# Kernel optimization log

Hardware: AMD Instinct MI355X
Metric: run time of the kernel (lower is better)

## Reference

```python
import jax, jax.numpy as jnp
import numpy as np

B, S, T, DIN, H, DOUT = 64, 256, 256, 128, 1024, 128
TEACHER_FORCING_RATIO = 0.0  # deterministic reference: always feed back own prediction


def setup_inputs() -> dict:
    key = jax.random.key(0)
    ks = jax.random.split(key, 12)
    bound = 1.0 / np.sqrt(H)
    u = lambda k, sh: jax.random.uniform(k, sh, jnp.float32, -bound, bound)
    return {
        "src": jax.random.normal(ks[0], (B, S, DIN), jnp.float32),
        "trg": jax.random.normal(ks[1], (B, T, DOUT), jnp.float32),
        "enc_Wih": u(ks[2], (4 * H, DIN)),
        "enc_Whh": u(ks[3], (4 * H, H)),
        "enc_bih": u(ks[4], (4 * H,)),
        "enc_bhh": u(ks[5], (4 * H,)),
        "dec_Wih": u(ks[6], (4 * H, DOUT)),
        "dec_Whh": u(ks[7], (4 * H, H)),
        "dec_bih": u(ks[8], (4 * H,)),
        "dec_bhh": u(ks[9], (4 * H,)),
        "fc_W": u(ks[10], (DOUT, H)),
        "fc_b": u(ks[11], (DOUT,)),
    }


def _lstm_cell(x_t, h, c, Wih, Whh, b):
    # PyTorch gate order: i, f, g, o
    gates = x_t @ Wih.T + h @ Whh.T + b  # [B, 4H]
    i, f, g, o = jnp.split(gates, 4, axis=-1)
    c = jax.nn.sigmoid(f) * c + jax.nn.sigmoid(i) * jnp.tanh(g)
    h = jax.nn.sigmoid(o) * jnp.tanh(c)
    return h, c


def _encode(src, Wih, Whh, b):
    Bn = src.shape[0]
    Hn = Whh.shape[1]
    h0 = jnp.zeros((Bn, Hn), src.dtype)
    c0 = jnp.zeros((Bn, Hn), src.dtype)

    def step(carry, xt):
        h, c = carry
        h, c = _lstm_cell(xt, h, c, Wih, Whh, b)
        return (h, c), None

    (h, c), _ = jax.lax.scan(step, (h0, c0), jnp.swapaxes(src, 0, 1))
    return h, c


def reference(src, trg, enc_Wih, enc_Whh, enc_bih, enc_bhh,
              dec_Wih, dec_Whh, dec_bih, dec_bhh, fc_W, fc_b):
    Bn, Tn, Dn = trg.shape
    h, c = _encode(src, enc_Wih, enc_Whh, enc_bih + enc_bhh)
    db = dec_bih + dec_bhh

    def step(carry, _):
        h, c, inp = carry
        h, c = _lstm_cell(inp, h, c, dec_Wih, dec_Whh, db)
        pred = h @ fc_W.T + fc_b  # [B, DOUT]
        # teacher_forcing_ratio = 0.0 -> next input is own prediction
        return (h, c, pred), pred

    _, preds = jax.lax.scan(step, (h, c, trg[:, 0, :]), None, length=Tn - 1)
    preds = jnp.swapaxes(preds, 0, 1)  # [B, T-1, DOUT]
    # outputs[:, 0, :] stays zero, as in the original
    return jnp.concatenate([jnp.zeros((Bn, 1, Dn), trg.dtype), preds], axis=1)
```

## Files before the change

### kernel.cpp

```cpp
#include <hip/hip_runtime.h>


#define BB   64
#define HH   1024
#define G4   4096
#define DXX  128
#define KC   128
#define SEQN 256
#define TN   256
#define OUT_BSTRIDE (TN * DXX)

#define HROW 2048
#define SLOT (64 * HROW)

typedef __attribute__((ext_vector_type(8))) short short8;
typedef __attribute__((ext_vector_type(4))) float f32x4;

__device__ __forceinline__ float sigm(float x)  { return 1.f / (1.f + __expf(-x)); }
__device__ __forceinline__ float tanh_f(float x){ return 1.f - 2.f / (1.f + __expf(2.f * x)); }

__device__ __forceinline__ unsigned short bf16_rn(float x) {
    union { float f; unsigned u; } v; v.f = x;
    unsigned r = v.u + 0x7fffu + ((v.u >> 16) & 1u);
    return (unsigned short)(r >> 16);
}
__device__ __forceinline__ float bf16f(unsigned short h) {
    union { unsigned u; float f; } v; v.u = ((unsigned)h) << 16; return v.f;
}

template<int KT, bool XPART>
__device__ __forceinline__ void do_step(
    const short8 (&w)[9][2],
    const unsigned short* __restrict__ A,
    unsigned short* __restrict__ An,
    float* red, int mrow, int kl, int kw, int rbase,
    int t, int b, int nl, int nh, const float (&bb)[4], float& creg,
    const unsigned short* __restrict__ xs,
    unsigned* __restrict__ bar, unsigned step)
{
    f32x4 acc = {0.f, 0.f, 0.f, 0.f};
    const unsigned short* Ar = A + mrow * HROW;
    #pragma unroll
    for (int kt = 0; kt < KT; ++kt) {
        const int kg = kw * (KT * 32) + kt * 32 + kl;
        short8 ah, al;
        if (XPART && kw == 3 && kt >= 5) {
            const int xo = mrow * 256 + (kg - 1024);
            ah = *(const short8*)(xs + xo);
            al = *(const short8*)(xs + xo + 128);
        } else {
            ah = *(const short8*)(Ar + kg);
            al = *(const short8*)(Ar + 1024 + kg);
        }
        acc = __builtin_amdgcn_mfma_f32_16x16x32_bf16(ah, w[kt][0], acc, 0, 0, 0);
        acc = __builtin_amdgcn_mfma_f32_16x16x32_bf16(ah, w[kt][1], acc, 0, 0, 0);
        acc = __builtin_amdgcn_mfma_f32_16x16x32_bf16(al, w[kt][0], acc, 0, 0, 0);
    }
    #pragma unroll
    for (int r = 0; r < 4; ++r) red[rbase + r * 17] = acc[r];
    __syncthreads();

    if (t < 256) {
        float g4[4];
        #pragma unroll
        for (int gt = 0; gt < 4; ++gt) {
            const int cc = nl * 4 + gt;
            g4[gt] = red[b * 17 + cc] + red[(64 + b) * 17 + cc]
                   + red[(128 + b) * 17 + cc] + red[(192 + b) * 17 + cc] + bb[gt];
        }
        const float cv = sigm(g4[1]) * creg + sigm(g4[0]) * tanh_f(g4[2]);
        creg = cv;
        const float hv = sigm(g4[3]) * tanh_f(cv);
        const unsigned short hh = bf16_rn(hv);
        const unsigned short hl = bf16_rn(hv - bf16f(hh));
        const unsigned phh = (unsigned)__shfl_xor((int)(unsigned)hh, 1);
        const unsigned phl = (unsigned)__shfl_xor((int)(unsigned)hl, 1);
        if ((nl & 1) == 0) {
            const unsigned wh = (unsigned)hh | (phh << 16);
            const unsigned wl = (unsigned)hl | (phl << 16);
            __hip_atomic_store((unsigned*)(An + b * HROW + nh), wh,
                               __ATOMIC_RELAXED, __HIP_MEMORY_SCOPE_AGENT);
            __hip_atomic_store((unsigned*)(An + b * HROW + 1024 + nh), wl,
                               __ATOMIC_RELAXED, __HIP_MEMORY_SCOPE_AGENT);
        }
    }
    __syncthreads();
    if (t == 0)
        __hip_atomic_store(bar + blockIdx.x, step,
                           __ATOMIC_RELAXED, __HIP_MEMORY_SCOPE_AGENT);
    if (blockIdx.x == 0) {
        if (t < 64) {
            const unsigned* sp = bar + t * 4;
            for (;;) {
                const unsigned m0 = __hip_atomic_load(sp + 0, __ATOMIC_RELAXED, __HIP_MEMORY_SCOPE_AGENT);
                const unsigned m1 = __hip_atomic_load(sp + 1, __ATOMIC_RELAXED, __HIP_MEMORY_SCOPE_AGENT);
                const unsigned m2 = __hip_atomic_load(sp + 2, __ATOMIC_RELAXED, __HIP_MEMORY_SCOPE_AGENT);
                const unsigned m3 = __hip_atomic_load(sp + 3, __ATOMIC_RELAXED, __HIP_MEMORY_SCOPE_AGENT);
                const bool ok = (m0 >= step) & (m1 >= step) & (m2 >= step) & (m3 >= step);
                if (__all((int)ok)) break;
                __builtin_amdgcn_s_sleep(1);
            }
            if (t < 16)
                __hip_atomic_store(bar + 256 + t * 32, step,
                                   __ATOMIC_RELAXED, __HIP_MEMORY_SCOPE_AGENT);
        }
    } else if (t == 0) {
        const unsigned* ep = bar + 256 + (blockIdx.x & 15) * 32;
        while (__hip_atomic_load(ep, __ATOMIC_RELAXED,
                                 __HIP_MEMORY_SCOPE_AGENT) < step)
            __builtin_amdgcn_s_sleep(1);
    }
    __syncthreads();
}

__global__ __launch_bounds__(1024, 1)
void persist(const unsigned short* __restrict__ Wencf,
             const unsigned short* __restrict__ Wdec0f,
             const unsigned short* __restrict__ Wcombf,
             const unsigned short* __restrict__ srcp,
             const unsigned short* __restrict__ trgp,
             const float* __restrict__ benc,
             const float* __restrict__ bdec0,
             const float* __restrict__ bcomb,
             unsigned short* __restrict__ hseq,
             unsigned* __restrict__ bar)
{
    __shared__ float red[4 * 64 * 17];
    const int t  = threadIdx.x;
    const int bi = blockIdx.x;
    const int l  = t & 63;
    const int wv = t >> 6;
    const int mw = wv & 3;
    const int kw = wv >> 2;
    const int lm = l & 15;
    const int kl = (l >> 4) << 3;
    const int mrow = mw * 16 + lm;
    const int rbase = (kw * 64 + mw * 16 + (l >> 4) * 4) * 17 + lm;
    const int b  = t >> 2;
    const int nl = t & 3;
    const int nh = bi * 4 + nl;

    short8 w[9][2];
    float bb[4];
    float creg = 0.f;
    unsigned step = 0;

    {
        const unsigned short* wp = Wencf + ((size_t)(bi * 4 + kw) * 9) * 1024 + l * 8;
        #pragma unroll
        for (int kt = 0; kt < 9; ++kt) {
            w[kt][0] = *(const short8*)(wp + kt * 1024);
            w[kt][1] = *(const short8*)(wp + kt * 1024 + 512);
            asm volatile("" : "+v"(w[kt][0]), "+v"(w[kt][1]));
        }
    }
    if (t < 256) {
        #pragma unroll
        for (int g = 0; g < 4; ++g) bb[g] = benc[bi * 16 + nl * 4 + g];
    }
    for (int s = 0; s < 256; ++s) {
        ++step;
        do_step<9, true>(w, hseq + (size_t)s * SLOT, hseq + (size_t)(s + 1) * SLOT,
                         red, mrow, kl, kw, rbase, t, b, nl, nh, bb, creg,
                         srcp + (size_t)s * 16384, bar, step);
    }
    {
        const unsigned short* wp = Wdec0f + ((size_t)(bi * 4 + kw) * 9) * 1024 + l * 8;
        #pragma unroll
        for (int kt = 0; kt < 9; ++kt) {
            w[kt][0] = *(const short8*)(wp + kt * 1024);
            w[kt][1] = *(const short8*)(wp + kt * 1024 + 512);
            asm volatile("" : "+v"(w[kt][0]), "+v"(w[kt][1]));
        }
    }
    if (t < 256) {
        #pragma unroll
        for (int g = 0; g < 4; ++g) bb[g] = bdec0[bi * 16 + nl * 4 + g];
    }
    ++step;
    do_step<9, true>(w, hseq + (size_t)256 * SLOT, hseq + (size_t)257 * SLOT,
                     red, mrow, kl, kw, rbase, t, b, nl, nh, bb, creg,
                     trgp, bar, step);
    {
        const unsigned short* wp = Wcombf + ((size_t)(bi * 4 + kw) * 8) * 1024 + l * 8;
        #pragma unroll
        for (int kt = 0; kt < 8; ++kt) {
            w[kt][0] = *(const short8*)(wp + kt * 1024);
            w[kt][1] = *(const short8*)(wp + kt * 1024 + 512);
            asm volatile("" : "+v"(w[kt][0]), "+v"(w[kt][1]));
        }
    }
    if (t < 256) {
        #pragma unroll
        for (int g = 0; g < 4; ++g) bb[g] = bcomb[bi * 16 + nl * 4 + g];
    }
    for (int s = 257; s < 511; ++s) {
        ++step;
        do_step<8, false>(w, hseq + (size_t)s * SLOT, hseq + (size_t)(s + 1) * SLOT,
                          red, mrow, kl, kw, rbase, t, b, nl, nh, bb, creg,
                          nullptr, bar, step);
    }
}

__global__ __launch_bounds__(256)
void fc_batch(const unsigned short* __restrict__ fcf,
              const unsigned short* __restrict__ hseq,
              const float* __restrict__ fcb,
              float* __restrict__ out)
{
    const int t = threadIdx.x, bi = blockIdx.x;
    const int l = t & 63, wv = t >> 6;
    const int lm = l & 15, kl = (l >> 4) << 3;
    const int mrow = wv * 16 + lm;
    const unsigned short* Ar = hseq + (size_t)(257 + bi) * SLOT + mrow * HROW;

    f32x4 acc[8];
    #pragma unroll
    for (int nt = 0; nt < 8; ++nt) acc[nt] = f32x4{0.f, 0.f, 0.f, 0.f};

    for (int kt = 0; kt < 32; ++kt) {
        const short8 ah = *(const short8*)(Ar + kt * 32 + kl);
        const short8 al = *(const short8*)(Ar + 1024 + kt * 32 + kl);
        #pragma unroll
        for (int nt = 0; nt < 8; ++nt) {
            const unsigned short* bp = fcf + (size_t)(nt * 32 + kt) * 1024 + l * 8;
            const short8 bh = *(const short8*)bp;
            const short8 bl = *(const short8*)(bp + 512);
            acc[nt] = __builtin_amdgcn_mfma_f32_16x16x32_bf16(ah, bh, acc[nt], 0, 0, 0);
            acc[nt] = __builtin_amdgcn_mfma_f32_16x16x32_bf16(ah, bl, acc[nt], 0, 0, 0);
            acc[nt] = __builtin_amdgcn_mfma_f32_16x16x32_bf16(al, bh, acc[nt], 0, 0, 0);
        }
    }
    #pragma unroll
    for (int nt = 0; nt < 8; ++nt) {
        const float bv = fcb[nt * 16 + lm];
        #pragma unroll
        for (int r = 0; r < 4; ++r) {
            const int bq = wv * 16 + (l >> 4) * 4 + r;
            out[(size_t)bq * OUT_BSTRIDE + (size_t)(bi + 1) * DXX + nt * 16 + lm] = acc[nt][r] + bv;
        }
    }
}

__global__ __launch_bounds__(256)
void prep_frag_12(const float* __restrict__ Whh, const float* __restrict__ Wih,
                  unsigned short* __restrict__ dst)
{
    const int idx = blockIdx.x * 256 + threadIdx.x;
    const int l = idx & 63;
    const int fid = idx >> 6;
    const int kt = fid % 9;
    const int rem = fid / 9;
    const int kw = rem & 3;
    const int biq = rem >> 2;
    const int col = biq * 16 + (l & 15);
    const int hid = col >> 2, g = col & 3;
    const int k0 = kw * 288 + kt * 32 + ((l >> 4) << 3);
    short8 vh, vl;
    #pragma unroll
    for (int e = 0; e < 8; ++e) {
        const int k = k0 + e;
        const float wv = (k < 1024) ? Whh[(size_t)(g * 1024 + hid) * 1024 + k]
                                    : Wih[(size_t)(g * 1024 + hid) * 128 + (k - 1024)];
        const unsigned short hi = bf16_rn(wv);
        vh[e] = (short)hi;
        vl[e] = (short)bf16_rn(wv - bf16f(hi));
    }
    *(short8*)(dst + (size_t)fid * 1024 + l * 8) = vh;
    *(short8*)(dst + (size_t)fid * 1024 + 512 + l * 8) = vl;
}

__global__ __launch_bounds__(256)
void prep_frag_comb(const float* __restrict__ Wc, unsigned short* __restrict__ dst)
{
    const int idx = blockIdx.x * 256 + threadIdx.x;
    const int l = idx & 63;
    const int fid = idx >> 6;
    const int kt = fid & 7;
    const int rem = fid >> 3;
    const int kw = rem & 3;
    const int biq = rem >> 2;
    const int col = biq * 16 + (l & 15);
    const int hid = col >> 2, g = col & 3;
    const int k0 = kw * 256 + kt * 32 + ((l >> 4) << 3);
    short8 vh, vl;
    #pragma unroll
    for (int e = 0; e < 8; ++e) {
        const float wv = Wc[(size_t)(g * 1024 + hid) * 1024 + k0 + e];
        const unsigned short hi = bf16_rn(wv);
        vh[e] = (short)hi;
        vl[e] = (short)bf16_rn(wv - bf16f(hi));
    }
    *(short8*)(dst + (size_t)fid * 1024 + l * 8) = vh;
    *(short8*)(dst + (size_t)fid * 1024 + 512 + l * 8) = vl;
}

__global__ __launch_bounds__(256)
void prep_frag_fc(const float* __restrict__ fcW, unsigned short* __restrict__ dst)
{
    const int idx = blockIdx.x * 256 + threadIdx.x;
    const int l = idx & 63;
    const int fid = idx >> 6;
    const int nt = fid >> 5, kt = fid & 31;
    const int col = nt * 16 + (l & 15);
    const int k0 = kt * 32 + ((l >> 4) << 3);
    short8 vh, vl;
    #pragma unroll
    for (int e = 0; e < 8; ++e) {
        const float wv = fcW[(size_t)col * 1024 + k0 + e];
        const unsigned short hi = bf16_rn(wv);
        vh[e] = (short)hi;
        vl[e] = (short)bf16_rn(wv - bf16f(hi));
    }
    *(short8*)(dst + (size_t)fid * 1024 + l * 8) = vh;
    *(short8*)(dst + (size_t)fid * 1024 + 512 + l * 8) = vl;
}

__global__ __launch_bounds__(256)
void prep_bias_p(const float* __restrict__ ebi, const float* __restrict__ ebh,
                 const float* __restrict__ dbi, const float* __restrict__ dbh,
                 const float* __restrict__ dWih, const float* __restrict__ fcb,
                 float* __restrict__ benc, float* __restrict__ bdec0,
                 float* __restrict__ bcomb)
{
    const int idx = blockIdx.x * 256 + threadIdx.x;
    const int orig = ((idx & 3) << 10) | (idx >> 2);
    benc[idx] = ebi[orig] + ebh[orig];
    const float db = dbi[orig] + dbh[orig];
    bdec0[idx] = db;
    float a = db;
    const float* wr = dWih + (size_t)orig * DXX;
    for (int d = 0; d < DXX; ++d) a += wr[d] * fcb[d];
    bcomb[idx] = a;
}

__global__ __launch_bounds__(256)
void prep_src(const float* __restrict__ src, unsigned short* __restrict__ so, int n)
{
    const int idx = blockIdx.x * 256 + threadIdx.x;
    if (idx < n) {
        const int b = idx >> 15, s = (idx >> 7) & 255, d = idx & 127;
        const float v = src[idx];
        const unsigned short hi = bf16_rn(v);
        unsigned short* dst = so + ((size_t)s * 64 + b) * 256 + d;
        dst[0]   = hi;
        dst[128] = bf16_rn(v - bf16f(hi));
    }
}

__global__ __launch_bounds__(256)
void prep_trg0(const float* __restrict__ trg, unsigned short* __restrict__ tp)
{
    const int idx = blockIdx.x * 256 + threadIdx.x;
    const int bq = idx >> 7, d = idx & 127;
    const float v = trg[(size_t)bq * TN * DXX + d];
    const unsigned short hi = bf16_rn(v);
    tp[bq * 256 + d] = hi;
    tp[bq * 256 + 128 + d] = bf16_rn(v - bf16f(hi));
}

__global__ __launch_bounds__(256)
void init_persist(unsigned short* __restrict__ hseq, float* __restrict__ out,
                  unsigned* __restrict__ bar)
{
    const int idx = blockIdx.x * 256 + threadIdx.x;
    if (idx < SLOT / 2) {
        ((unsigned*)hseq)[idx] = 0u;
    } else if (idx < SLOT / 2 + BB * DXX) {
        const int r = idx - SLOT / 2;
        out[(size_t)(r >> 7) * OUT_BSTRIDE + (r & 127)] = 0.f;
    } else if (idx < SLOT / 2 + BB * DXX + 2048) {
        __hip_atomic_store(bar + (idx - (SLOT / 2 + BB * DXX)), 0u,
                           __ATOMIC_RELAXED, __HIP_MEMORY_SCOPE_AGENT);
    }
}

__global__ __launch_bounds__(256)
void step_kernel(const float* __restrict__ W, const float* __restrict__ Wx,
                 const float* __restrict__ x, int xstride,
                 const float* __restrict__ bias,
                 const float* __restrict__ h_in, float* __restrict__ c,
                 float* __restrict__ h_out, int nGates,
                 const float* __restrict__ fcW, const float* __restrict__ fcb,
                 float* __restrict__ fc_out, float* __restrict__ predbuf)
{
    __shared__ float hT[KC][BB + 1];
    __shared__ float wl[16][KC];
    const int t   = threadIdx.x;
    const int b   = t & 63;
    const int q   = t >> 6;
    const int col = t & (KC - 1);
    const int r0  = t >> 7;
    const int bi  = blockIdx.x;

    if (bi < nGates) {
        const int n0 = bi * 4;
        const int n  = n0 + q;
        float a0 = bias[n], a1 = bias[HH + n], a2 = bias[2 * HH + n], a3 = bias[3 * HH + n];
        for (int k0 = 0; k0 < HH; k0 += KC) {
            #pragma unroll
            for (int rr = 0; rr < BB; rr += 2)
                hT[col][rr + r0] = h_in[(rr + r0) * HH + k0 + col];
            #pragma unroll
            for (int rr = 0; rr < 16; rr += 2) {
                const int r = rr + r0;
                const int j = (r & 3) * HH + n0 + (r >> 2);
                wl[r][col] = W[(size_t)j * HH + k0 + col];
            }
            __syncthreads();
            #pragma unroll 8
            for (int k = 0; k < KC; k += 4) {
                const float4 w0 = *reinterpret_cast<const float4*>(&wl[q * 4 + 0][k]);
                const float4 w1 = *reinterpret_cast<const float4*>(&wl[q * 4 + 1][k]);
                const float4 w2 = *reinterpret_cast<const float4*>(&wl[q * 4 + 2][k]);
                const float4 w3 = *reinterpret_cast<const float4*>(&wl[q * 4 + 3][k]);
                const float h0v = hT[k][b], h1v = hT[k + 1][b];
                const float h2v = hT[k + 2][b], h3v = hT[k + 3][b];
                a0 += h0v * w0.x + h1v * w0.y + h2v * w0.z + h3v * w0.w;
                a1 += h0v * w1.x + h1v * w1.y + h2v * w1.z + h3v * w1.w;
                a2 += h0v * w2.x + h1v * w2.y + h2v * w2.z + h3v * w2.w;
                a3 += h0v * w3.x + h1v * w3.y + h2v * w3.z + h3v * w3.w;
            }
            __syncthreads();
        }
        if (Wx != nullptr) {
            #pragma unroll
            for (int rr = 0; rr < BB; rr += 2)
                hT[col][rr + r0] = x[(size_t)(rr + r0) * xstride + col];
            #pragma unroll
            for (int rr = 0; rr < 16; rr += 2) {
                const int r = rr + r0;
                const int j = (r & 3) * HH + n0 + (r >> 2);
                wl[r][col] = Wx[(size_t)j * DXX + col];
            }
            __syncthreads();
            #pragma unroll 8
            for (int k = 0; k < DXX; k += 4) {
                const float4 w0 = *reinterpret_cast<const float4*>(&wl[q * 4 + 0][k]);
                const float4 w1 = *reinterpret_cast<const float4*>(&wl[q * 4 + 1][k]);
                const float4 w2 = *reinterpret_cast<const float4*>(&wl[q * 4 + 2][k]);
                const float4 w3 = *reinterpret_cast<const float4*>(&wl[q * 4 + 3][k]);
                const float h0v = hT[k][b], h1v = hT[k + 1][b];
                const float h2v = hT[k + 2][b], h3v = hT[k + 3][b];
                a0 += h0v * w0.x + h1v * w0.y + h2v * w0.z + h3v * w0.w;
                a1 += h0v * w1.x + h1v * w1.y + h2v * w1.z + h3v * w1.w;
                a2 += h0v * w2.x + h1v * w2.y + h2v * w2.z + h3v * w2.w;
                a3 += h0v * w3.x + h1v * w3.y + h2v * w3.z + h3v * w3.w;
            }
        }
        const int ci = b * HH + n;
        const float cv = sigm(a1) * c[ci] + sigm(a0) * tanh_f(a2);
        c[ci] = cv;
        h_out[ci] = sigm(a3) * tanh_f(cv);
    } else if (fcW != nullptr && bi < nGates + 32) {
        const int d0 = (bi - nGates) * 4;
        float a = 0.f;
        for (int k0 = 0; k0 < HH; k0 += KC) {
            #pragma unroll
            for (int rr = 0; rr < BB; rr += 2)
                hT[col][rr + r0] = h_in[(rr + r0) * HH + k0 + col];
            #pragma unroll
            for (int rr = 0; rr < 4; rr += 2)
                wl[rr + r0][col] = fcW[(size_t)(d0 + rr + r0) * HH + k0 + col];
            __syncthreads();
            #pragma unroll 8
            for (int k = 0; k < KC; k += 4) {
                const float4 w0 = *reinterpret_cast<const float4*>(&wl[q][k]);
                const float h0v = hT[k][b], h1v = hT[k + 1][b];
                const float h2v = hT[k + 2][b], h3v = hT[k + 3][b];
                a += h0v * w0.x + h1v * w0.y + h2v * w0.z + h3v * w0.w;
            }
            __syncthreads();
        }
        const int d = d0 + q;
        a += fcb[d];
        if (fc_out)  fc_out[(size_t)b * OUT_BSTRIDE + d] = a;
        if (predbuf) predbuf[b * DXX + d] = a;
    }
}

__global__ __launch_bounds__(256)
void bias_prep(const float* __restrict__ ebi, const float* __restrict__ ebh,
               const float* __restrict__ dbi, const float* __restrict__ dbh,
               const float* __restrict__ dWih, const float* __restrict__ fcbv,
               float* __restrict__ enc_b, float* __restrict__ dec_b, float* __restrict__ bcomb)
{
    __shared__ float fb[DXX];
    const int t = threadIdx.x;
    const int j = blockIdx.x * 256 + t;
    if (t < DXX) fb[t] = fcbv[t];
    __syncthreads();
    enc_b[j] = ebi[j] + ebh[j];
    const float db = dbi[j] + dbh[j];
    dec_b[j] = db;
    float acc = db;
    const float* wr = dWih + (size_t)j * DXX;
    for (int d = 0; d < DXX; d += 4) {
        const float4 w = *reinterpret_cast<const float4*>(&wr[d]);
        acc += w.x * fb[d] + w.y * fb[d + 1] + w.z * fb[d + 2] + w.w * fb[d + 3];
    }
    bcomb[j] = acc;
}

__global__ __launch_bounds__(256)
void wcomb_kernel(const float* __restrict__ dWhh, const float* __restrict__ dWih,
                  const float* __restrict__ fcW, float* __restrict__ Wcomb)
{
    const int bi = blockIdx.x;
    const int j0 = (bi >> 2) * 8;
    const int n  = (bi & 3) * 256 + threadIdx.x;
    __shared__ float wih[8][DXX];
    for (int i = threadIdx.x; i < 8 * DXX; i += 256)
        wih[i >> 7][i & 127] = dWih[(size_t)(j0 + (i >> 7)) * DXX + (i & 127)];
    __syncthreads();
    float acc[8];
    #pragma unroll
    for (int jj = 0; jj < 8; ++jj) acc[jj] = dWhh[(size_t)(j0 + jj) * HH + n];
    for (int d = 0; d < DXX; ++d) {
        const float fv = fcW[(size_t)d * HH + n];
        #pragma unroll
        for (int jj = 0; jj < 8; ++jj) acc[jj] += wih[jj][d] * fv;
    }
    #pragma unroll
    for (int jj = 0; jj < 8; ++jj) Wcomb[(size_t)(j0 + jj) * HH + n] = acc[jj];
}

__global__ __launch_bounds__(256)
void init_kernel(float* __restrict__ h0, float* __restrict__ c, float* __restrict__ out)
{
    const int idx = blockIdx.x * 256 + threadIdx.x;
    if (idx < BB * HH) h0[idx] = 0.f;
    else if (idx < 2 * BB * HH) c[idx - BB * HH] = 0.f;
    else {
        const int r = idx - 2 * BB * HH;
        if (r < BB * DXX) out[(size_t)(r >> 7) * OUT_BSTRIDE + (r & 127)] = 0.f;
    }
}

extern "C" void kernel_launch(void* const* d_in, const int* in_sizes, int n_in,
                              void* d_out, int out_size, void* d_ws, size_t ws_size,
                              hipStream_t stream) {
    const float* src   = (const float*)d_in[0];
    const float* trg   = (const float*)d_in[1];
    const float* eWih  = (const float*)d_in[2];
    const float* eWhh  = (const float*)d_in[3];
    const float* ebih  = (const float*)d_in[4];
    const float* ebhh  = (const float*)d_in[5];
    const float* dWih  = (const float*)d_in[6];
    const float* dWhh  = (const float*)d_in[7];
    const float* dbih  = (const float*)d_in[8];
    const float* dbhh  = (const float*)d_in[9];
    const float* fcW   = (const float*)d_in[10];
    const float* fcb   = (const float*)d_in[11];
    float* out = (float*)d_out;

    uintptr_t base = (uintptr_t)d_ws;
    size_t off = 0;
    auto alloc = [&](size_t bytes) -> void* {
        void* p = (void*)(base + off);
        off = (off + bytes + 255) & ~(size_t)255;
        return p;
    };
    unsigned* bar = (unsigned*)alloc(8192);
    unsigned short* srcp = (unsigned short*)alloc((size_t)SEQN * 64 * 256 * 2);
    unsigned short* trgp = (unsigned short*)alloc((size_t)64 * 256 * 2);
    float* benc  = (float*)alloc(G4 * 4);
    float* bdec0 = (float*)alloc(G4 * 4);
    float* bcomb = (float*)alloc(G4 * 4);
    unsigned short* fcf    = (unsigned short*)alloc((size_t)256 * 1024 * 2);
    unsigned short* Wencf  = (unsigned short*)alloc((size_t)9216 * 1024 * 2);
    unsigned short* Wdec0f = (unsigned short*)alloc((size_t)9216 * 1024 * 2);
    unsigned short* Wcombf = (unsigned short*)alloc((size_t)8192 * 1024 * 2);
    float* Wcomb32 = (float*)alloc((size_t)G4 * HH * 4);
    unsigned short* hseq   = (unsigned short*)alloc((size_t)512 * SLOT * 2);
    const bool fastok = (off <= ws_size);

    if (fastok) {
        init_persist<<<296, 256, 0, stream>>>(hseq, out, bar);
        prep_src<<<8192, 256, 0, stream>>>(src, srcp, BB * SEQN * DXX);
        prep_trg0<<<32, 256, 0, stream>>>(trg, trgp);
        prep_bias_p<<<16, 256, 0, stream>>>(ebih, ebhh, dbih, dbhh, dWih, fcb,
                                            benc, bdec0, bcomb);
        prep_frag_12<<<2304, 256, 0, stream>>>(eWhh, eWih, Wencf);
        prep_frag_12<<<2304, 256, 0, stream>>>(dWhh, dWih, Wdec0f);
        wcomb_kernel<<<2048, 256, 0, stream>>>(dWhh, dWih, fcW, Wcomb32);
        prep_frag_comb<<<2048, 256, 0, stream>>>(Wcomb32, Wcombf);
        prep_frag_fc<<<64, 256, 0, stream>>>(fcW, fcf);

        persist<<<256, 1024, 0, stream>>>(Wencf, Wdec0f, Wcombf, srcp, trgp,
                                          benc, bdec0, bcomb, hseq, bar);
        fc_batch<<<255, 256, 0, stream>>>(fcf, hseq, fcb, out);
        return;
    }

    float* ws  = (float*)d_ws;
    float* h0     = ws;
    float* h1     = ws + 65536;
    float* cF     = ws + 131072;
    float* pred   = ws + 196608;
    float* enc_b  = ws + 204800;
    float* dec_b  = ws + 208896;
    float* bcombF = ws + 212992;
    float* Wcomb  = ws + 217088;
    const bool use_comb = ws_size >= (size_t)(217088 + 4096 * 1024) * sizeof(float);

    init_kernel<<<544, 256, 0, stream>>>(h0, cF, out);
    bias_prep<<<16, 256, 0, stream>>>(ebih, ebhh, dbih, dbhh, dWih, fcb, enc_b, dec_b, bcombF);
    if (use_comb)
        wcomb_kernel<<<2048, 256, 0, stream>>>(dWhh, dWih, fcW, Wcomb);

    float* hc = h0;
    float* hn = h1;
    for (int s = 0; s < SEQN; ++s) {
        step_kernel<<<256, 256, 0, stream>>>(eWhh, eWih, src + s * DXX, SEQN * DXX,
                                             enc_b, hc, cF, hn, 256,
                                             nullptr, nullptr, nullptr, nullptr);
        float* tmp = hc; hc = hn; hn = tmp;
    }
    step_kernel<<<256, 256, 0, stream>>>(dWhh, dWih, trg, TN * DXX,
                                         dec_b, hc, cF, hn, 256,
                                         nullptr, nullptr, nullptr, nullptr);
    { float* tmp = hc; hc = hn; hn = tmp; }
    if (use_comb) {
        for (int tt = 1; tt <= TN - 2; ++tt) {
            step_kernel<<<288, 256, 0, stream>>>(Wcomb, nullptr, nullptr, 0,
                                                 bcombF, hc, cF, hn, 256,
                                                 fcW, fcb, out + (size_t)tt * DXX, nullptr);
            float* tmp = hc; hc = hn; hn = tmp;
        }
    } else {
        for (int tt = 1; tt <= TN - 2; ++tt) {
            step_kernel<<<32, 256, 0, stream>>>(nullptr, nullptr, nullptr, 0,
                                                nullptr, hc, nullptr, nullptr, 0,
                                                fcW, fcb, out + (size_t)tt * DXX, pred);
            step_kernel<<<256, 256, 0, stream>>>(dWhh, dWih, pred, DXX,
                                                 dec_b, hc, cF, hn, 256,
                                                 nullptr, nullptr, nullptr, nullptr);
            float* tmp = hc; hc = hn; hn = tmp;
        }
    }
    step_kernel<<<32, 256, 0, stream>>>(nullptr, nullptr, nullptr, 0,
                                        nullptr, hc, nullptr, nullptr, 0,
                                        fcW, fcb, out + (size_t)(TN - 1) * DXX, nullptr);
}
```

Before: 5.138 ms.

## Halve persistent grid to 128 blocks, holding second weight tile in LDS

Each persistent block now computes 32 gate columns instead of 16. One weight slice stays in registers and the other is staged into dynamic LDS, which is read with per-k-step loads feeding a second accumulator. Halving the block count cuts the participants in the grid-wide barrier and the number of redundant reads of the shared h state per step. In exchange each step does twice the MFMA work per block plus LDS traffic, and the barrier master scans fewer flags. The LDS request of roughly 105 KB per block must fit alongside one block per CU.

New measurement: 5.416 ms. 1.05x slower.

```diff
diff --git a/kernel.cpp b/kernel.cpp
--- a/kernel.cpp
+++ b/kernel.cpp
@@ -12,6 +12,9 @@
 
 #define HROW 2048
 #define SLOT (64 * HROW)
+#define WLDS_BYTES 73728
+#define RED_OFF 73728
+#define LDS_TOTAL (73728 + 4 * 64 * 33 * 4)
 
 typedef __attribute__((ext_vector_type(8))) short short8;
 typedef __attribute__((ext_vector_type(4))) float f32x4;
@@ -33,12 +36,20 @@
     const short8 (&w)[9][2],
     const unsigned short* __restrict__ A,
     unsigned short* __restrict__ An,
-    float* red, int mrow, int kl, int kw, int rbase,
-    int t, int b, int nl, int nh, const float (&bb)[4], float& creg,
+    int mrow, int kl, int kw,
+    int t, int b, int q, int nhb, const float (&bb)[4], float& creg,
     const unsigned short* __restrict__ xs,
     unsigned* __restrict__ bar, unsigned step)
 {
-    f32x4 acc = {0.f, 0.f, 0.f, 0.f};
+    extern __shared__ unsigned char ldsraw[];
+    const unsigned short* wl = (const unsigned short*)ldsraw;
+    float* red = (float*)(ldsraw + RED_OFF);
+
+    const int l  = t & 63;
+    const int lm = l & 15;
+
+    f32x4 accA = {0.f, 0.f, 0.f, 0.f};
+    f32x4 accB = {0.f, 0.f, 0.f, 0.f};
     const unsigned short* Ar = A + mrow * HROW;
     #pragma unroll
     for (int kt = 0; kt < KT; ++kt) {
@@ -52,21 +63,33 @@
             ah = *(const short8*)(Ar + kg);
             al = *(const short8*)(Ar + 1024 + kg);
         }
-        acc = __builtin_amdgcn_mfma_f32_16x16x32_bf16(ah, w[kt][0], acc, 0, 0, 0);
-        acc = __builtin_amdgcn_mfma_f32_16x16x32_bf16(ah, w[kt][1], acc, 0, 0, 0);
-        acc = __builtin_amdgcn_mfma_f32_16x16x32_bf16(al, w[kt][0], acc, 0, 0, 0);
-    }
-    #pragma unroll
-    for (int r = 0; r < 4; ++r) red[rbase + r * 17] = acc[r];
-    __syncthreads();
-
-    if (t < 256) {
+        const int wb = (kw * KT + kt) * 1024 + l * 8;
+        const short8 bhB = *(const short8*)(wl + wb);
+        const short8 blB = *(const short8*)(wl + wb + 512);
+        accA = __builtin_amdgcn_mfma_f32_16x16x32_bf16(ah, w[kt][0], accA, 0, 0, 0);
+        accA = __builtin_amdgcn_mfma_f32_16x16x32_bf16(ah, w[kt][1], accA, 0, 0, 0);
+        accA = __builtin_amdgcn_mfma_f32_16x16x32_bf16(al, w[kt][0], accA, 0, 0, 0);
+        accB = __builtin_amdgcn_mfma_f32_16x16x32_bf16(ah, bhB, accB, 0, 0, 0);
+        accB = __builtin_amdgcn_mfma_f32_16x16x32_bf16(ah, blB, accB, 0, 0, 0);
+        accB = __builtin_amdgcn_mfma_f32_16x16x32_bf16(al, bhB, accB, 0, 0, 0);
+    }
+    {
+        const int rb = (kw * 64 + mrow - lm + (l >> 4) * 4) * 33 + lm;
+        #pragma unroll
+        for (int r = 0; r < 4; ++r) {
+            red[rb + r * 33]      = accA[r];
+            red[rb + r * 33 + 16] = accB[r];
+        }
+    }
+    __syncthreads();
+
+    if (t < 512) {
         float g4[4];
         #pragma unroll
-        for (int gt = 0; gt < 4; ++gt) {
-            const int cc = nl * 4 + gt;
-            g4[gt] = red[b * 17 + cc] + red[(64 + b) * 17 + cc]
-                   + red[(128 + b) * 17 + cc] + red[(192 + b) * 17 + cc] + bb[gt];
+        for (int g = 0; g < 4; ++g) {
+            const int c = q * 4 + g;
+            g4[g] = red[b * 33 + c] + red[(64 + b) * 33 + c]
+                  + red[(128 + b) * 33 + c] + red[(192 + b) * 33 + c] + bb[g];
         }
         const float cv = sigm(g4[1]) * creg + sigm(g4[0]) * tanh_f(g4[2]);
         creg = cv;
@@ -75,12 +98,12 @@
         const unsigned short hl = bf16_rn(hv - bf16f(hh));
         const unsigned phh = (unsigned)__shfl_xor((int)(unsigned)hh, 1);
         const unsigned phl = (unsigned)__shfl_xor((int)(unsigned)hl, 1);
-        if ((nl & 1) == 0) {
+        if ((q & 1) == 0) {
             const unsigned wh = (unsigned)hh | (phh << 16);
-            const unsigned wl = (unsigned)hl | (phl << 16);
-            __hip_atomic_store((unsigned*)(An + b * HROW + nh), wh,
+            const unsigned wlv = (unsigned)hl | (phl << 16);
+            __hip_atomic_store((unsigned*)(An + b * HROW + nhb), wh,
                                __ATOMIC_RELAXED, __HIP_MEMORY_SCOPE_AGENT);
-            __hip_atomic_store((unsigned*)(An + b * HROW + 1024 + nh), wl,
+            __hip_atomic_store((unsigned*)(An + b * HROW + 1024 + nhb), wlv,
                                __ATOMIC_RELAXED, __HIP_MEMORY_SCOPE_AGENT);
         }
     }
@@ -90,13 +113,11 @@
                            __ATOMIC_RELAXED, __HIP_MEMORY_SCOPE_AGENT);
     if (blockIdx.x == 0) {
         if (t < 64) {
-            const unsigned* sp = bar + t * 4;
+            const unsigned* sp = bar + t * 2;
             for (;;) {
                 const unsigned m0 = __hip_atomic_load(sp + 0, __ATOMIC_RELAXED, __HIP_MEMORY_SCOPE_AGENT);
                 const unsigned m1 = __hip_atomic_load(sp + 1, __ATOMIC_RELAXED, __HIP_MEMORY_SCOPE_AGENT);
-                const unsigned m2 = __hip_atomic_load(sp + 2, __ATOMIC_RELAXED, __HIP_MEMORY_SCOPE_AGENT);
-                const unsigned m3 = __hip_atomic_load(sp + 3, __ATOMIC_RELAXED, __HIP_MEMORY_SCOPE_AGENT);
-                const bool ok = (m0 >= step) & (m1 >= step) & (m2 >= step) & (m3 >= step);
+                const bool ok = (m0 >= step) & (m1 >= step);
                 if (__all((int)ok)) break;
                 __builtin_amdgcn_s_sleep(1);
             }
@@ -111,6 +132,14 @@
             __builtin_amdgcn_s_sleep(1);
     }
     __syncthreads();
+}
+
+__device__ __forceinline__ void stage_wlds(const unsigned short* __restrict__ g, int nunits, int t)
+{
+    extern __shared__ unsigned char ldsraw[];
+    unsigned short* wl = (unsigned short*)ldsraw;
+    for (int u = t; u < nunits; u += 1024)
+        *(short8*)(wl + u * 8) = *(const short8*)(g + u * 8);
 }
 
 __global__ __launch_bounds__(1024, 1)
@@ -125,7 +154,6 @@
              unsigned short* __restrict__ hseq,
              unsigned* __restrict__ bar)
 {
-    __shared__ float red[4 * 64 * 17];
     const int t  = threadIdx.x;
     const int bi = blockIdx.x;
     const int l  = t & 63;
@@ -135,10 +163,9 @@
     const int lm = l & 15;
     const int kl = (l >> 4) << 3;
     const int mrow = mw * 16 + lm;
-    const int rbase = (kw * 64 + mw * 16 + (l >> 4) * 4) * 17 + lm;
-    const int b  = t >> 2;
-    const int nl = t & 3;
-    const int nh = bi * 4 + nl;
+    const int b  = t >> 3;
+    const int q  = t & 7;
+    const int nhb = bi * 8 + q;
 
     short8 w[9][2];
     float bb[4];
@@ -146,59 +173,63 @@
     unsigned step = 0;
 
     {
-        const unsigned short* wp = Wencf + ((size_t)(bi * 4 + kw) * 9) * 1024 + l * 8;
+        const unsigned short* wp = Wencf + ((size_t)(2 * bi) * 36 + kw * 9) * 1024 + l * 8;
         #pragma unroll
         for (int kt = 0; kt < 9; ++kt) {
             w[kt][0] = *(const short8*)(wp + kt * 1024);
             w[kt][1] = *(const short8*)(wp + kt * 1024 + 512);
             asm volatile("" : "+v"(w[kt][0]), "+v"(w[kt][1]));
         }
-    }
-    if (t < 256) {
-        #pragma unroll
-        for (int g = 0; g < 4; ++g) bb[g] = benc[bi * 16 + nl * 4 + g];
-    }
+        stage_wlds(Wencf + (size_t)(2 * bi + 1) * 36 * 1024, 36 * 128, t);
+    }
+    if (t < 512) {
+        #pragma unroll
+        for (int g = 0; g < 4; ++g) bb[g] = benc[bi * 32 + q * 4 + g];
+    }
+    __syncthreads();
     for (int s = 0; s < 256; ++s) {
         ++step;
         do_step<9, true>(w, hseq + (size_t)s * SLOT, hseq + (size_t)(s + 1) * SLOT,
-                         red, mrow, kl, kw, rbase, t, b, nl, nh, bb, creg,
+                         mrow, kl, kw, t, b, q, nhb, bb, creg,
                          srcp + (size_t)s * 16384, bar, step);
     }
     {
-        const unsigned short* wp = Wdec0f + ((size_t)(bi * 4 + kw) * 9) * 1024 + l * 8;
+        const unsigned short* wp = Wdec0f + ((size_t)(2 * bi) * 36 + kw * 9) * 1024 + l * 8;
         #pragma unroll
         for (int kt = 0; kt < 9; ++kt) {
             w[kt][0] = *(const short8*)(wp + kt * 1024);
             w[kt][1] = *(const short8*)(wp + kt * 1024 + 512);
             asm volatile("" : "+v"(w[kt][0]), "+v"(w[kt][1]));
         }
-    }
-    if (t < 256) {
-        #pragma unroll
-        for (int g = 0; g < 4; ++g) bb[g] = bdec0[bi * 16 + nl * 4 + g];
-    }
+        stage_wlds(Wdec0f + (size_t)(2 * bi + 1) * 36 * 1024, 36 * 128, t);
+    }
+    if (t < 512) {
+        #pragma unroll
+        for (int g = 0; g < 4; ++g) bb[g] = bdec0[bi * 32 + q * 4 + g];
+    }
+    __syncthreads();
     ++step;
     do_step<9, true>(w, hseq + (size_t)256 * SLOT, hseq + (size_t)257 * SLOT,
-                     red, mrow, kl, kw, rbase, t, b, nl, nh, bb, creg,
-                     trgp, bar, step);
+                     mrow, kl, kw, t, b, q, nhb, bb, creg, trgp, bar, step);
     {
-        const unsigned short* wp = Wcombf + ((size_t)(bi * 4 + kw) * 8) * 1024 + l * 8;
+        const unsigned short* wp = Wcombf + ((size_t)(2 * bi) * 32 + kw * 8) * 1024 + l * 8;
         #pragma unroll
         for (int kt = 0; kt < 8; ++kt) {
             w[kt][0] = *(const short8*)(wp + kt * 1024);
             w[kt][1] = *(const short8*)(wp + kt * 1024 + 512);
             asm volatile("" : "+v"(w[kt][0]), "+v"(w[kt][1]));
         }
-    }
-    if (t < 256) {
-        #pragma unroll
-        for (int g = 0; g < 4; ++g) bb[g] = bcomb[bi * 16 + nl * 4 + g];
-    }
+        stage_wlds(Wcombf + (size_t)(2 * bi + 1) * 32 * 1024, 32 * 128, t);
+    }
+    if (t < 512) {
+        #pragma unroll
+        for (int g = 0; g < 4; ++g) bb[g] = bcomb[bi * 32 + q * 4 + g];
+    }
+    __syncthreads();
     for (int s = 257; s < 511; ++s) {
         ++step;
         do_step<8, false>(w, hseq + (size_t)s * SLOT, hseq + (size_t)(s + 1) * SLOT,
-                          red, mrow, kl, kw, rbase, t, b, nl, nh, bb, creg,
-                          nullptr, bar, step);
+                          mrow, kl, kw, t, b, q, nhb, bb, creg, nullptr, bar, step);
     }
 }
 
@@ -587,8 +618,8 @@
         prep_frag_comb<<<2048, 256, 0, stream>>>(Wcomb32, Wcombf);
         prep_frag_fc<<<64, 256, 0, stream>>>(fcW, fcf);
 
-        persist<<<256, 1024, 0, stream>>>(Wencf, Wdec0f, Wcombf, srcp, trgp,
-                                          benc, bdec0, bcomb, hseq, bar);
+        persist<<<128, 1024, LDS_TOTAL, stream>>>(Wencf, Wdec0f, Wcombf, srcp, trgp,
+                                                  benc, bdec0, bcomb, hseq, bar);
         fc_batch<<<255, 256, 0, stream>>>(fcf, hseq, fcb, out);
         return;
     }
```
